# Kernel tuning notes

Hardware: AMD Instinct MI355X
Metric: run time of the kernel (lower is better)

Reference implementation:

```python
import jax, jax.numpy as jnp
import numpy as np


def setup_inputs() -> dict:
    key = jax.random.key(0)
    k1, k2, k3, k4 = jax.random.split(key, 4)
    B, C, H, Wd = 32, 512, 32, 32
    sparse_dim, dict_size, feature_dim = 1024, 1024, 512
    x = jax.random.normal(k1, (B, C, H, Wd), dtype=jnp.float32)
    dictionary = jax.random.normal(k2, (dict_size, feature_dim), dtype=jnp.float32)
    # scale W, S like the LISTA init (|| . || ~ O(1)) so iterates stay bounded
    W = jax.random.normal(k3, (sparse_dim, feature_dim), dtype=jnp.float32) * 0.02
    S = jax.random.normal(k4, (sparse_dim, sparse_dim), dtype=jnp.float32) * 0.02
    thresh = jnp.float32(0.1)
    return {"x": x, "dictionary": dictionary, "W": W, "S": S, "thresh": thresh, "num_steps": 5}


def _soft_threshold(z, thresh):
    return jnp.sign(z) * jnp.maximum(jnp.abs(z) - thresh, 0.0)


def reference(x, dictionary, W, S, thresh, num_steps):
    B, C, H, Wd = x.shape
    sparse_dim = S.shape[0]
    # [B,C,H,W] -> [B*H*W, C]
    x_flat = jnp.transpose(x, (0, 2, 3, 1)).reshape(-1, C)
    dict_norm = dictionary / jnp.linalg.norm(dictionary, axis=1, keepdims=True)
    # W @ x^T is loop-invariant; compute once. [K, N]
    Wx = W @ x_flat.T
    z = jnp.zeros((sparse_dim, x_flat.shape[0]), dtype=x.dtype)
    for _ in range(num_steps):
        z = z + Wx
        z = z - S @ z
        z = _soft_threshold(z, thresh)
    # [K,N] -> [B,K,H,W]
    z = jnp.transpose(z.T.reshape(B, H, Wd, sparse_dim), (0, 3, 1, 2))
    return (z, dict_norm)
```

## Files before the change

### kernel.cpp

```cpp
#include <hip/hip_runtime.h>
#include <hip/hip_bf16.h>

typedef __bf16 bf16_t;
typedef __bf16 bf16x8 __attribute__((ext_vector_type(8)));
typedef float f32x4 __attribute__((ext_vector_type(4)));

#define GLOAD_LDS16(g, l)                                                      \
  __builtin_amdgcn_global_load_lds(                                            \
      (const __attribute__((address_space(1))) void*)(g),                      \
      (__attribute__((address_space(3))) void*)(l), 16, 0, 0)

#define MFMA(a, b, c) __builtin_amdgcn_mfma_f32_16x16x32_bf16((a), (b), (c), 0, 0, 0)

__global__ __launch_bounds__(512, 2) void gemm8_kernel(
    const bf16_t* __restrict__ A, const bf16_t* __restrict__ Bt,
    int Kd, int mode,
    const bf16_t* __restrict__ WxIn, bf16_t* __restrict__ UnextOrWx,
    float* __restrict__ Out, const float* __restrict__ thresh_p)
{
  __shared__ __align__(16) char smem[131072];
  bf16_t* lds = (bf16_t*)smem;

  const int tid  = threadIdx.x;
  const int wid  = tid >> 6, lane = tid & 63;
  const int wr = wid >> 2, wc = wid & 3;
  const int lr = lane & 15, kg = lane >> 4;
  const int l2 = lane >> 2, l4 = lane & 3;

  const int per     = gridDim.x >> 3;
  const int logical = (blockIdx.x & 7) * per + (blockIdx.x >> 3);
  const int tileN = (logical & 3) << 8;
  const int tileM = (logical >> 2) << 8;

  const int NT = Kd >> 6;

  auto stageA = [&](int t, int h, int buf) {
    const int k0 = t << 6;
    #pragma unroll
    for (int l = 0; l < 2; ++l) {
      const int c  = l * 8 + wid;
      const int ks = c >> 3, c3 = c & 7, q = c3 >> 2;
      const int R  = q * 128 + h * 64 + (c3 & 3) * 16 + l2;
      const int kcs = l4 ^ ((R >> 1) & 3);
      const bf16_t* src = A + (size_t)(tileM + R) * Kd + k0 + ks * 32 + kcs * 8;
      bf16_t* dst = lds + buf * 32768 + ks * 8192 + q * 4096 + h * 2048 + (c3 & 3) * 512;
      GLOAD_LDS16(src, dst);
    }
  };
  auto stageB = [&](int t, int g, int buf) {
    const int k0 = t << 6;
    #pragma unroll
    for (int l = 0; l < 2; ++l) {
      const int c  = l * 8 + wid;
      const int ks = c >> 3, c3 = c & 7, q2 = c3 >> 1;
      const int R  = q2 * 64 + g * 32 + (c3 & 1) * 16 + l2;
      const int kcs = l4 ^ ((R >> 1) & 3);
      const bf16_t* src = Bt + (size_t)(tileN + R) * Kd + k0 + ks * 32 + kcs * 8;
      bf16_t* dst = lds + buf * 32768 + 16384 + ks * 8192 + q2 * 2048 + g * 1024 + (c3 & 1) * 512;
      GLOAD_LDS16(src, dst);
    }
  };
  auto readA = [&](int mi, int ks, int buf) -> bf16x8 {
    const int R = wr * 128 + mi * 16 + lr;
    return *(const bf16x8*)(lds + buf * 32768 + ks * 8192 + R * 32 + ((kg ^ ((R >> 1) & 3)) << 3));
  };
  auto readB = [&](int ni, int ks, int buf) -> bf16x8 {
    const int R = wc * 64 + ni * 16 + lr;
    return *(const bf16x8*)(lds + buf * 32768 + 16384 + ks * 8192 + R * 32 + ((kg ^ ((R >> 1) & 3)) << 3));
  };

  f32x4 acc[8][4] = {};
  bf16x8 af[4][2], b0[2][2], b1[2][2];

  stageA(0, 0, 0); stageB(0, 0, 0); stageB(0, 1, 0); stageA(0, 1, 0);
  asm volatile("s_waitcnt vmcnt(4)" ::: "memory");
  __builtin_amdgcn_s_barrier();

  for (int t = 0; t < NT; ++t) {
    const int cur = t & 1, nxt = cur ^ 1;
    const int tn = (t + 1 == NT) ? 0 : t + 1;

    #pragma unroll
    for (int mi = 0; mi < 4; ++mi) { af[mi][0] = readA(mi, 0, cur); af[mi][1] = readA(mi, 1, cur); }
    #pragma unroll
    for (int ni = 0; ni < 2; ++ni) { b0[ni][0] = readB(ni, 0, cur); b0[ni][1] = readB(ni, 1, cur); }
    stageA(tn, 0, nxt);
    __builtin_amdgcn_s_barrier();
    asm volatile("s_waitcnt lgkmcnt(0)" ::: "memory");
    __builtin_amdgcn_sched_barrier(0);
    __builtin_amdgcn_s_setprio(1);
    #pragma unroll
    for (int mi = 0; mi < 4; ++mi)
      #pragma unroll
      for (int ni = 0; ni < 2; ++ni) {
        acc[mi][ni] = MFMA(af[mi][0], b0[ni][0], acc[mi][ni]);
        acc[mi][ni] = MFMA(af[mi][1], b0[ni][1], acc[mi][ni]);
      }
    __builtin_amdgcn_s_setprio(0);
    asm volatile("s_waitcnt vmcnt(4)" ::: "memory");
    __builtin_amdgcn_s_barrier();

    #pragma unroll
    for (int ni = 0; ni < 2; ++ni) { b1[ni][0] = readB(ni + 2, 0, cur); b1[ni][1] = readB(ni + 2, 1, cur); }
    stageB(tn, 0, nxt);
    __builtin_amdgcn_s_barrier();
    asm volatile("s_waitcnt lgkmcnt(0)" ::: "memory");
    __builtin_amdgcn_sched_barrier(0);
    __builtin_amdgcn_s_setprio(1);
    #pragma unroll
    for (int mi = 0; mi < 4; ++mi)
      #pragma unroll
      for (int ni = 0; ni < 2; ++ni) {
        acc[mi][ni + 2] = MFMA(af[mi][0], b1[ni][0], acc[mi][ni + 2]);
        acc[mi][ni + 2] = MFMA(af[mi][1], b1[ni][1], acc[mi][ni + 2]);
      }
    __builtin_amdgcn_s_setprio(0);
    asm volatile("s_waitcnt vmcnt(4)" ::: "memory");
    __builtin_amdgcn_s_barrier();

    #pragma unroll
    for (int mi = 0; mi < 4; ++mi) { af[mi][0] = readA(mi + 4, 0, cur); af[mi][1] = readA(mi + 4, 1, cur); }
    stageB(tn, 1, nxt);
    __builtin_amdgcn_s_barrier();
    asm volatile("s_waitcnt lgkmcnt(0)" ::: "memory");
    __builtin_amdgcn_sched_barrier(0);
    __builtin_amdgcn_s_setprio(1);
    #pragma unroll
    for (int mi = 0; mi < 4; ++mi)
      #pragma unroll
      for (int ni = 0; ni < 2; ++ni) {
        acc[mi + 4][ni + 2] = MFMA(af[mi][0], b1[ni][0], acc[mi + 4][ni + 2]);
        acc[mi + 4][ni + 2] = MFMA(af[mi][1], b1[ni][1], acc[mi + 4][ni + 2]);
      }
    __builtin_amdgcn_s_setprio(0);
    __builtin_amdgcn_s_barrier();

    stageA(tn, 1, nxt);
    __builtin_amdgcn_s_barrier();
    __builtin_amdgcn_s_setprio(1);
    #pragma unroll
    for (int mi = 0; mi < 4; ++mi)
      #pragma unroll
      for (int ni = 0; ni < 2; ++ni) {
        acc[mi + 4][ni] = MFMA(af[mi][0], b0[ni][0], acc[mi + 4][ni]);
        acc[mi + 4][ni] = MFMA(af[mi][1], b0[ni][1], acc[mi + 4][ni]);
      }
    __builtin_amdgcn_s_setprio(0);
    asm volatile("s_waitcnt vmcnt(4)" ::: "memory");
    __builtin_amdgcn_s_barrier();
  }

  const float th = *thresh_p;

  if (mode == 0) {
    #pragma unroll
    for (int mi = 0; mi < 8; ++mi)
      #pragma unroll
      for (int ni = 0; ni < 4; ++ni) {
        const int row0 = tileM + wr * 128 + mi * 16 + kg * 4;
        const int col  = tileN + wc * 64 + ni * 16 + lr;
        #pragma unroll
        for (int r = 0; r < 4; ++r)
          UnextOrWx[(size_t)(row0 + r) * 1024 + col] = (bf16_t)acc[mi][ni][r];
      }
  } else if (mode == 1) {
    #pragma unroll
    for (int mi = 0; mi < 8; ++mi)
      #pragma unroll
      for (int ni = 0; ni < 4; ++ni) {
        const int row0 = tileM + wr * 128 + mi * 16 + kg * 4;
        const int col  = tileN + wc * 64 + ni * 16 + lr;
        #pragma unroll
        for (int r = 0; r < 4; ++r) {
          const size_t idx = (size_t)(row0 + r) * 1024 + col;
          const float u  = (float)A[idx];
          const float wx = (float)WxIn[idx];
          const float tt = u - acc[mi][ni][r];
          const float a  = fabsf(tt) - th;
          const float zn = (a > 0.f) ? copysignf(a, tt) : 0.f;
          UnextOrWx[idx] = (bf16_t)(zn + wx);
        }
      }
  } else {
    #pragma unroll
    for (int mi = 0; mi < 8; ++mi)
      #pragma unroll
      for (int ni = 0; ni < 4; ++ni) {
        const int row0 = tileM + wr * 128 + mi * 16 + kg * 4;
        const int col  = tileN + wc * 64 + ni * 16 + lr;
        #pragma unroll
        for (int r = 0; r < 4; ++r) {
          const size_t idx = (size_t)(row0 + r) * 1024 + col;
          const float u  = (float)A[idx];
          const float tt = u - acc[mi][ni][r];
          const float a  = fabsf(tt) - th;
          acc[mi][ni][r] = (a > 0.f) ? copysignf(a, tt) : 0.f;
        }
      }
    asm volatile("s_waitcnt vmcnt(0)" ::: "memory");
    __syncthreads();
    float* T = (float*)smem;
    const int    bb    = tileM >> 10;
    const size_t obase = (size_t)bb * 1048576 + (size_t)(tileM & 1023);
    for (int ch = 0; ch < 8; ++ch) {
      if (ch) __syncthreads();
      if (wc == (ch >> 1)) {
        #pragma unroll
        for (int nj = 0; nj < 2; ++nj) {
          const int ni = (ch & 1) * 2 + nj;
          const int cp = nj * 16 + lr;
          #pragma unroll
          for (int mi = 0; mi < 8; ++mi)
            #pragma unroll
            for (int r = 0; r < 4; ++r)
              T[cp * 260 + wr * 128 + mi * 16 + kg * 4 + r] = acc[mi][ni][r];
        }
      }
      __syncthreads();
      #pragma unroll
      for (int j = 0; j < 4; ++j) {
        const int f  = tid + j * 512;
        const int cp = f >> 6;
        const int R4 = (f & 63) * 4;
        const f32x4 v = *(const f32x4*)&T[cp * 260 + R4];
        *(f32x4*)&Out[obase + (size_t)(tileN + ch * 32 + cp) * 1024 + R4] = v;
      }
    }
  }
}

__global__ void cast_f32_bf16_kernel(const float* __restrict__ src,
                                     bf16_t* __restrict__ dst, int n) {
  int i = blockIdx.x * blockDim.x + threadIdx.x;
  if (i < n) dst[i] = (bf16_t)src[i];
}

__global__ void transpose_cast_x_kernel(const float* __restrict__ x,
                                        bf16_t* __restrict__ xt) {
  __shared__ float t[32][33];
  const int b  = blockIdx.z;
  const int p0 = blockIdx.x * 32;
  const int c0 = blockIdx.y * 32;
  const int tx = threadIdx.x, ty = threadIdx.y;
  #pragma unroll
  for (int i = 0; i < 32; i += 8)
    t[ty + i][tx] = x[((size_t)b * 512 + c0 + ty + i) * 1024 + p0 + tx];
  __syncthreads();
  #pragma unroll
  for (int i = 0; i < 32; i += 8)
    xt[((size_t)b * 1024 + p0 + ty + i) * 512 + c0 + tx] = (bf16_t)t[tx][ty + i];
}

__global__ void dict_norm_kernel(const float* __restrict__ dict,
                                 float* __restrict__ out) {
  const int row = blockIdx.x;
  const int tid = threadIdx.x;
  const float* r = dict + (size_t)row * 512;
  float s = 0.f;
  for (int i = tid; i < 512; i += 256) { float v = r[i]; s += v * v; }
  #pragma unroll
  for (int off = 32; off > 0; off >>= 1) s += __shfl_down(s, off);
  __shared__ float ps[4];
  if ((tid & 63) == 0) ps[tid >> 6] = s;
  __syncthreads();
  const float inv = 1.0f / sqrtf(ps[0] + ps[1] + ps[2] + ps[3]);
  for (int i = tid; i < 512; i += 256) out[(size_t)row * 512 + i] = r[i] * inv;
}

extern "C" void kernel_launch(void* const* d_in, const int* in_sizes, int n_in,
                              void* d_out, int out_size, void* d_ws, size_t ws_size,
                              hipStream_t stream) {
  const float* x      = (const float*)d_in[0];
  const float* dict   = (const float*)d_in[1];
  const float* W      = (const float*)d_in[2];
  const float* S      = (const float*)d_in[3];
  const float* thresh = (const float*)d_in[4];

  float* out = (float*)d_out;

  char* ws = (char*)d_ws;
  bf16_t* uA   = (bf16_t*)ws;
  bf16_t* uB   = (bf16_t*)(ws + 67108864);
  bf16_t* WxBf = (bf16_t*)(ws + 134217728);
  bf16_t* xt   = (bf16_t*)(ws + 201326592);
  bf16_t* Wbf  = (bf16_t*)(ws + 234881024);
  bf16_t* Sbf  = (bf16_t*)(ws + 235929600);

  float* dnorm = out + 33554432;

  cast_f32_bf16_kernel<<<dim3(2048), dim3(256), 0, stream>>>(W, Wbf, 524288);
  cast_f32_bf16_kernel<<<dim3(4096), dim3(256), 0, stream>>>(S, Sbf, 1048576);
  transpose_cast_x_kernel<<<dim3(32, 16, 32), dim3(32, 8), 0, stream>>>(x, xt);
  dict_norm_kernel<<<dim3(1024), dim3(256), 0, stream>>>(dict, dnorm);

  gemm8_kernel<<<dim3(512), dim3(512), 0, stream>>>(
      xt, Wbf, 512, 0, nullptr, WxBf, nullptr, thresh);

  bf16_t* uc = WxBf; bf16_t* un = uA;
  for (int s = 0; s < 4; ++s) {
    gemm8_kernel<<<dim3(512), dim3(512), 0, stream>>>(
        uc, Sbf, 1024, 1, WxBf, un, nullptr, thresh);
    uc = un;
    un = (uc == uA) ? uB : uA;
  }
  gemm8_kernel<<<dim3(512), dim3(512), 0, stream>>>(
      uc, Sbf, 1024, 2, nullptr, nullptr, out, thresh);
}
```

Measured before the change: 626.3 us.

## Fold identity into S matrix and shrink GEMM tile to 128x256

Replaces S with T = I - S so that u - S·u becomes a single GEMM u·T^T. This drops the epilogue reload of the A operand (u) in modes 1 and 2. The GEMM tile also shrinks from 256x256 to 128x256 with a K-step of 32 and 48KB of LDS, doubling the grid to 1024 blocks and targeting 4 blocks per CU. The cost is smaller per-block reuse and more barriers per unit of work, and folding the identity into bf16 T changes rounding slightly.

```diff
diff --git a/kernel.cpp b/kernel.cpp
--- a/kernel.cpp
+++ b/kernel.cpp
@@ -12,191 +12,146 @@
 
 #define MFMA(a, b, c) __builtin_amdgcn_mfma_f32_16x16x32_bf16((a), (b), (c), 0, 0, 0)
 
-__global__ __launch_bounds__(512, 2) void gemm8_kernel(
+__global__ __launch_bounds__(512, 4) void gemm_kernel(
     const bf16_t* __restrict__ A, const bf16_t* __restrict__ Bt,
     int Kd, int mode,
     const bf16_t* __restrict__ WxIn, bf16_t* __restrict__ UnextOrWx,
     float* __restrict__ Out, const float* __restrict__ thresh_p)
 {
-  __shared__ __align__(16) char smem[131072];
+  __shared__ __align__(16) char smem[49152];
   bf16_t* lds = (bf16_t*)smem;
 
-  const int tid  = threadIdx.x;
-  const int wid  = tid >> 6, lane = tid & 63;
+  const int tid = threadIdx.x;
+  const int wid = tid >> 6, lane = tid & 63;
   const int wr = wid >> 2, wc = wid & 3;
   const int lr = lane & 15, kg = lane >> 4;
-  const int l2 = lane >> 2, l4 = lane & 3;
-
-  const int per     = gridDim.x >> 3;
+
+  const int per = gridDim.x >> 3;
   const int logical = (blockIdx.x & 7) * per + (blockIdx.x >> 3);
   const int tileN = (logical & 3) << 8;
-  const int tileM = (logical >> 2) << 8;
-
-  const int NT = Kd >> 6;
-
-  auto stageA = [&](int t, int h, int buf) {
-    const int k0 = t << 6;
-    #pragma unroll
-    for (int l = 0; l < 2; ++l) {
-      const int c  = l * 8 + wid;
-      const int ks = c >> 3, c3 = c & 7, q = c3 >> 2;
-      const int R  = q * 128 + h * 64 + (c3 & 3) * 16 + l2;
-      const int kcs = l4 ^ ((R >> 1) & 3);
-      const bf16_t* src = A + (size_t)(tileM + R) * Kd + k0 + ks * 32 + kcs * 8;
-      bf16_t* dst = lds + buf * 32768 + ks * 8192 + q * 4096 + h * 2048 + (c3 & 3) * 512;
-      GLOAD_LDS16(src, dst);
-    }
+  const int tileM = (logical >> 2) << 7;
+  const int NT = Kd >> 5;
+
+  const int l4 = tid & 3, t2 = tid >> 2;
+  const int rowA = t2;
+  const int kcsA = l4 ^ ((rowA >> 1) & 3);
+  const size_t offA = (size_t)(tileM + rowA) * Kd + kcsA * 8;
+
+  auto stageA = [&](int t, int buf) {
+    GLOAD_LDS16(A + offA + (t << 5), lds + buf * 12288 + tid * 8);
   };
   auto stageB = [&](int t, int g, int buf) {
-    const int k0 = t << 6;
-    #pragma unroll
-    for (int l = 0; l < 2; ++l) {
-      const int c  = l * 8 + wid;
-      const int ks = c >> 3, c3 = c & 7, q2 = c3 >> 1;
-      const int R  = q2 * 64 + g * 32 + (c3 & 1) * 16 + l2;
-      const int kcs = l4 ^ ((R >> 1) & 3);
-      const bf16_t* src = Bt + (size_t)(tileN + R) * Kd + k0 + ks * 32 + kcs * 8;
-      bf16_t* dst = lds + buf * 32768 + 16384 + ks * 8192 + q2 * 2048 + g * 1024 + (c3 & 1) * 512;
-      GLOAD_LDS16(src, dst);
-    }
-  };
-  auto readA = [&](int mi, int ks, int buf) -> bf16x8 {
-    const int R = wr * 128 + mi * 16 + lr;
-    return *(const bf16x8*)(lds + buf * 32768 + ks * 8192 + R * 32 + ((kg ^ ((R >> 1) & 3)) << 3));
-  };
-  auto readB = [&](int ni, int ks, int buf) -> bf16x8 {
-    const int R = wc * 64 + ni * 16 + lr;
-    return *(const bf16x8*)(lds + buf * 32768 + 16384 + ks * 8192 + R * 32 + ((kg ^ ((R >> 1) & 3)) << 3));
-  };
-
-  f32x4 acc[8][4] = {};
-  bf16x8 af[4][2], b0[2][2], b1[2][2];
-
-  stageA(0, 0, 0); stageB(0, 0, 0); stageB(0, 1, 0); stageA(0, 1, 0);
-  asm volatile("s_waitcnt vmcnt(4)" ::: "memory");
+    const int col = (t2 >> 5) * 64 + g * 32 + (t2 & 31);
+    const int kcs = l4 ^ ((col >> 1) & 3);
+    GLOAD_LDS16(Bt + (size_t)(tileN + col) * Kd + (t << 5) + kcs * 8,
+                lds + buf * 12288 + 4096 + col * 32 + l4 * 8);
+  };
+  auto readA = [&](int mi, int buf) -> bf16x8 {
+    const int R = wr * 64 + mi * 16 + lr;
+    return *(const bf16x8*)(lds + buf * 12288 + R * 32 + ((kg ^ ((R >> 1) & 3)) << 3));
+  };
+  auto readB = [&](int ni, int buf) -> bf16x8 {
+    const int C = wc * 64 + ni * 16 + lr;
+    return *(const bf16x8*)(lds + buf * 12288 + 4096 + C * 32 + ((kg ^ ((C >> 1) & 3)) << 3));
+  };
+
+  f32x4 acc[4][4] = {};
+  bf16x8 af[2], b0[2], b1[2];
+
+  stageA(0, 0); stageB(0, 0, 0); stageB(0, 1, 0);
+  asm volatile("s_waitcnt vmcnt(1)" ::: "memory");
   __builtin_amdgcn_s_barrier();
 
   for (int t = 0; t < NT; ++t) {
     const int cur = t & 1, nxt = cur ^ 1;
     const int tn = (t + 1 == NT) ? 0 : t + 1;
 
-    #pragma unroll
-    for (int mi = 0; mi < 4; ++mi) { af[mi][0] = readA(mi, 0, cur); af[mi][1] = readA(mi, 1, cur); }
-    #pragma unroll
-    for (int ni = 0; ni < 2; ++ni) { b0[ni][0] = readB(ni, 0, cur); b0[ni][1] = readB(ni, 1, cur); }
-    stageA(tn, 0, nxt);
-    __builtin_amdgcn_s_barrier();
+    af[0] = readA(0, cur); af[1] = readA(1, cur);
+    b0[0] = readB(0, cur); b0[1] = readB(1, cur);
+    stageA(tn, nxt);
     asm volatile("s_waitcnt lgkmcnt(0)" ::: "memory");
     __builtin_amdgcn_sched_barrier(0);
     __builtin_amdgcn_s_setprio(1);
+    acc[0][0] = MFMA(af[0], b0[0], acc[0][0]);
+    acc[0][1] = MFMA(af[0], b0[1], acc[0][1]);
+    acc[1][0] = MFMA(af[1], b0[0], acc[1][0]);
+    acc[1][1] = MFMA(af[1], b0[1], acc[1][1]);
+    __builtin_amdgcn_s_setprio(0);
+    asm volatile("s_waitcnt vmcnt(1)" ::: "memory");
+    __builtin_amdgcn_s_barrier();
+
+    b1[0] = readB(2, cur); b1[1] = readB(3, cur);
+    stageB(tn, 0, nxt);
+    asm volatile("s_waitcnt lgkmcnt(0)" ::: "memory");
+    __builtin_amdgcn_sched_barrier(0);
+    __builtin_amdgcn_s_setprio(1);
+    acc[0][2] = MFMA(af[0], b1[0], acc[0][2]);
+    acc[0][3] = MFMA(af[0], b1[1], acc[0][3]);
+    acc[1][2] = MFMA(af[1], b1[0], acc[1][2]);
+    acc[1][3] = MFMA(af[1], b1[1], acc[1][3]);
+    __builtin_amdgcn_s_setprio(0);
+
+    af[0] = readA(2, cur); af[1] = readA(3, cur);
+    stageB(tn, 1, nxt);
+    asm volatile("s_waitcnt lgkmcnt(0)" ::: "memory");
+    __builtin_amdgcn_sched_barrier(0);
+    __builtin_amdgcn_s_setprio(1);
+    acc[2][2] = MFMA(af[0], b1[0], acc[2][2]);
+    acc[2][3] = MFMA(af[0], b1[1], acc[2][3]);
+    acc[3][2] = MFMA(af[1], b1[0], acc[3][2]);
+    acc[3][3] = MFMA(af[1], b1[1], acc[3][3]);
+    __builtin_amdgcn_s_setprio(0);
+
+    __builtin_amdgcn_s_setprio(1);
+    acc[2][0] = MFMA(af[0], b0[0], acc[2][0]);
+    acc[2][1] = MFMA(af[0], b0[1], acc[2][1]);
+    acc[3][0] = MFMA(af[1], b0[0], acc[3][0]);
+    acc[3][1] = MFMA(af[1], b0[1], acc[3][1]);
+    __builtin_amdgcn_s_setprio(0);
+    asm volatile("s_waitcnt vmcnt(1)" ::: "memory");
+    __builtin_amdgcn_s_barrier();
+  }
+
+  const float th = *thresh_p;
+
+  if (mode == 0) {
     #pragma unroll
     for (int mi = 0; mi < 4; ++mi)
       #pragma unroll
-      for (int ni = 0; ni < 2; ++ni) {
-        acc[mi][ni] = MFMA(af[mi][0], b0[ni][0], acc[mi][ni]);
-        acc[mi][ni] = MFMA(af[mi][1], b0[ni][1], acc[mi][ni]);
-      }
-    __builtin_amdgcn_s_setprio(0);
-    asm volatile("s_waitcnt vmcnt(4)" ::: "memory");
-    __builtin_amdgcn_s_barrier();
-
-    #pragma unroll
-    for (int ni = 0; ni < 2; ++ni) { b1[ni][0] = readB(ni + 2, 0, cur); b1[ni][1] = readB(ni + 2, 1, cur); }
-    stageB(tn, 0, nxt);
-    __builtin_amdgcn_s_barrier();
-    asm volatile("s_waitcnt lgkmcnt(0)" ::: "memory");
-    __builtin_amdgcn_sched_barrier(0);
-    __builtin_amdgcn_s_setprio(1);
+      for (int ni = 0; ni < 4; ++ni) {
+        const int row0 = tileM + wr * 64 + mi * 16 + kg * 4;
+        const int col  = tileN + wc * 64 + ni * 16 + lr;
+        #pragma unroll
+        for (int r = 0; r < 4; ++r)
+          UnextOrWx[(size_t)(row0 + r) * 1024 + col] = (bf16_t)acc[mi][ni][r];
+      }
+  } else if (mode == 1) {
     #pragma unroll
     for (int mi = 0; mi < 4; ++mi)
       #pragma unroll
-      for (int ni = 0; ni < 2; ++ni) {
-        acc[mi][ni + 2] = MFMA(af[mi][0], b1[ni][0], acc[mi][ni + 2]);
-        acc[mi][ni + 2] = MFMA(af[mi][1], b1[ni][1], acc[mi][ni + 2]);
-      }
-    __builtin_amdgcn_s_setprio(0);
-    asm volatile("s_waitcnt vmcnt(4)" ::: "memory");
-    __builtin_amdgcn_s_barrier();
-
-    #pragma unroll
-    for (int mi = 0; mi < 4; ++mi) { af[mi][0] = readA(mi + 4, 0, cur); af[mi][1] = readA(mi + 4, 1, cur); }
-    stageB(tn, 1, nxt);
-    __builtin_amdgcn_s_barrier();
-    asm volatile("s_waitcnt lgkmcnt(0)" ::: "memory");
-    __builtin_amdgcn_sched_barrier(0);
-    __builtin_amdgcn_s_setprio(1);
+      for (int ni = 0; ni < 4; ++ni) {
+        const int row0 = tileM + wr * 64 + mi * 16 + kg * 4;
+        const int col  = tileN + wc * 64 + ni * 16 + lr;
+        #pragma unroll
+        for (int r = 0; r < 4; ++r) {
+          const size_t idx = (size_t)(row0 + r) * 1024 + col;
+          const float v  = acc[mi][ni][r];
+          const float a  = fabsf(v) - th;
+          const float zn = (a > 0.f) ? copysignf(a, v) : 0.f;
+          UnextOrWx[idx] = (bf16_t)(zn + (float)WxIn[idx]);
+        }
+      }
+  } else {
     #pragma unroll
     for (int mi = 0; mi < 4; ++mi)
       #pragma unroll
-      for (int ni = 0; ni < 2; ++ni) {
-        acc[mi + 4][ni + 2] = MFMA(af[mi][0], b1[ni][0], acc[mi + 4][ni + 2]);
-        acc[mi + 4][ni + 2] = MFMA(af[mi][1], b1[ni][1], acc[mi + 4][ni + 2]);
-      }
-    __builtin_amdgcn_s_setprio(0);
-    __builtin_amdgcn_s_barrier();
-
-    stageA(tn, 1, nxt);
-    __builtin_amdgcn_s_barrier();
-    __builtin_amdgcn_s_setprio(1);
-    #pragma unroll
-    for (int mi = 0; mi < 4; ++mi)
-      #pragma unroll
-      for (int ni = 0; ni < 2; ++ni) {
-        acc[mi + 4][ni] = MFMA(af[mi][0], b0[ni][0], acc[mi + 4][ni]);
-        acc[mi + 4][ni] = MFMA(af[mi][1], b0[ni][1], acc[mi + 4][ni]);
-      }
-    __builtin_amdgcn_s_setprio(0);
-    asm volatile("s_waitcnt vmcnt(4)" ::: "memory");
-    __builtin_amdgcn_s_barrier();
-  }
-
-  const float th = *thresh_p;
-
-  if (mode == 0) {
-    #pragma unroll
-    for (int mi = 0; mi < 8; ++mi)
-      #pragma unroll
-      for (int ni = 0; ni < 4; ++ni) {
-        const int row0 = tileM + wr * 128 + mi * 16 + kg * 4;
-        const int col  = tileN + wc * 64 + ni * 16 + lr;
-        #pragma unroll
-        for (int r = 0; r < 4; ++r)
-          UnextOrWx[(size_t)(row0 + r) * 1024 + col] = (bf16_t)acc[mi][ni][r];
-      }
-  } else if (mode == 1) {
-    #pragma unroll
-    for (int mi = 0; mi < 8; ++mi)
-      #pragma unroll
-      for (int ni = 0; ni < 4; ++ni) {
-        const int row0 = tileM + wr * 128 + mi * 16 + kg * 4;
-        const int col  = tileN + wc * 64 + ni * 16 + lr;
+      for (int ni = 0; ni < 4; ++ni)
         #pragma unroll
         for (int r = 0; r < 4; ++r) {
-          const size_t idx = (size_t)(row0 + r) * 1024 + col;
-          const float u  = (float)A[idx];
-          const float wx = (float)WxIn[idx];
-          const float tt = u - acc[mi][ni][r];
-          const float a  = fabsf(tt) - th;
-          const float zn = (a > 0.f) ? copysignf(a, tt) : 0.f;
-          UnextOrWx[idx] = (bf16_t)(zn + wx);
+          const float v = acc[mi][ni][r];
+          const float a = fabsf(v) - th;
+          acc[mi][ni][r] = (a > 0.f) ? copysignf(a, v) : 0.f;
         }
-      }
-  } else {
-    #pragma unroll
-    for (int mi = 0; mi < 8; ++mi)
-      #pragma unroll
-      for (int ni = 0; ni < 4; ++ni) {
-        const int row0 = tileM + wr * 128 + mi * 16 + kg * 4;
-        const int col  = tileN + wc * 64 + ni * 16 + lr;
-        #pragma unroll
-        for (int r = 0; r < 4; ++r) {
-          const size_t idx = (size_t)(row0 + r) * 1024 + col;
-          const float u  = (float)A[idx];
-          const float tt = u - acc[mi][ni][r];
-          const float a  = fabsf(tt) - th;
-          acc[mi][ni][r] = (a > 0.f) ? copysignf(a, tt) : 0.f;
-        }
-      }
     asm volatile("s_waitcnt vmcnt(0)" ::: "memory");
     __syncthreads();
     float* T = (float*)smem;
@@ -210,19 +165,19 @@
           const int ni = (ch & 1) * 2 + nj;
           const int cp = nj * 16 + lr;
           #pragma unroll
-          for (int mi = 0; mi < 8; ++mi)
+          for (int mi = 0; mi < 4; ++mi)
             #pragma unroll
             for (int r = 0; r < 4; ++r)
-              T[cp * 260 + wr * 128 + mi * 16 + kg * 4 + r] = acc[mi][ni][r];
+              T[cp * 132 + wr * 64 + mi * 16 + kg * 4 + r] = acc[mi][ni][r];
         }
       }
       __syncthreads();
       #pragma unroll
-      for (int j = 0; j < 4; ++j) {
+      for (int j = 0; j < 2; ++j) {
         const int f  = tid + j * 512;
-        const int cp = f >> 6;
-        const int R4 = (f & 63) * 4;
-        const f32x4 v = *(const f32x4*)&T[cp * 260 + R4];
+        const int cp = f >> 5;
+        const int R4 = (f & 31) * 4;
+        const f32x4 v = *(const f32x4*)&T[cp * 132 + R4];
         *(f32x4*)&Out[obase + (size_t)(tileN + ch * 32 + cp) * 1024 + R4] = v;
       }
     }
@@ -233,6 +188,13 @@
                                      bf16_t* __restrict__ dst, int n) {
   int i = blockIdx.x * blockDim.x + threadIdx.x;
   if (i < n) dst[i] = (bf16_t)src[i];
+}
+
+__global__ void make_T_kernel(const float* __restrict__ S,
+                              bf16_t* __restrict__ T) {
+  const int idx = blockIdx.x * blockDim.x + threadIdx.x;
+  const int i = idx >> 10, j = idx & 1023;
+  T[idx] = (bf16_t)(((i == j) ? 1.0f : 0.0f) - S[idx]);
 }
 
 __global__ void transpose_cast_x_kernel(const float* __restrict__ x,
@@ -284,25 +246,25 @@
   bf16_t* WxBf = (bf16_t*)(ws + 134217728);
   bf16_t* xt   = (bf16_t*)(ws + 201326592);
   bf16_t* Wbf  = (bf16_t*)(ws + 234881024);
-  bf16_t* Sbf  = (bf16_t*)(ws + 235929600);
+  bf16_t* Tbf  = (bf16_t*)(ws + 235929600);
 
   float* dnorm = out + 33554432;
 
   cast_f32_bf16_kernel<<<dim3(2048), dim3(256), 0, stream>>>(W, Wbf, 524288);
-  cast_f32_bf16_kernel<<<dim3(4096), dim3(256), 0, stream>>>(S, Sbf, 1048576);
+  make_T_kernel<<<dim3(2048), dim3(512), 0, stream>>>(S, Tbf);
   transpose_cast_x_kernel<<<dim3(32, 16, 32), dim3(32, 8), 0, stream>>>(x, xt);
   dict_norm_kernel<<<dim3(1024), dim3(256), 0, stream>>>(dict, dnorm);
 
-  gemm8_kernel<<<dim3(512), dim3(512), 0, stream>>>(
+  gemm_kernel<<<dim3(1024), dim3(512), 0, stream>>>(
       xt, Wbf, 512, 0, nullptr, WxBf, nullptr, thresh);
 
   bf16_t* uc = WxBf; bf16_t* un = uA;
   for (int s = 0; s < 4; ++s) {
-    gemm8_kernel<<<dim3(512), dim3(512), 0, stream>>>(
-        uc, Sbf, 1024, 1, WxBf, un, nullptr, thresh);
+    gemm_kernel<<<dim3(1024), dim3(512), 0, stream>>>(
+        uc, Tbf, 1024, 1, WxBf, un, nullptr, thresh);
     uc = un;
     un = (uc == uA) ? uB : uA;
   }
-  gemm8_kernel<<<dim3(512), dim3(512), 0, stream>>>(
-      uc, Sbf, 1024, 2, nullptr, nullptr, out, thresh);
-}
+  gemm_kernel<<<dim3(1024), dim3(512), 0, stream>>>(
+      uc, Tbf, 1024, 2, nullptr, nullptr, out, thresh);
+}
```

Result: no change. 627.8 us (+0.2%).
